# Optimization experiments

Hardware: AMD Instinct MI355X
Metric: run time of the kernel (lower is better)

Reference implementation:

```python
import jax, jax.numpy as jnp
import numpy as np
import math

N_EMBD = 2048
N_HEAD = 16
HEAD_DIM = N_EMBD // N_HEAD
B, T = 2, 2048


def setup_inputs() -> dict:
    key = jax.random.key(0)
    k1, k2, k3 = jax.random.split(key, 3)
    x = jax.random.normal(k1, (B, T, N_EMBD), dtype=jnp.float32)
    # Linear weights stored torch-style [out, in]; applied as x @ W.T
    W_gate = jax.random.normal(k2, (N_HEAD, N_EMBD), dtype=jnp.float32) * 0.02
    W_qkv = jax.random.normal(k3, (3 * N_EMBD, N_EMBD), dtype=jnp.float32) * 0.02
    return {"x": x, "W_gate": W_gate, "W_qkv": W_qkv}


def reference(x, W_gate, W_qkv):
    Bb, Tt, C = x.shape
    H, hd = N_HEAD, HEAD_DIM
    # --- top-1 head gating ---
    gating = jax.nn.softmax(x @ W_gate.T, axis=-1)            # [B,T,H]
    idx = jnp.argmax(gating, axis=-1)                          # [B,T]
    indicator = jax.nn.one_hot(idx, H, dtype=gating.dtype)     # [B,T,H] (no grad, like scatter of ones)
    top1_val = jnp.max(gating, axis=-1, keepdims=True)         # [B,T,1]
    gating_top1 = indicator * top1_val                         # [B,T,H]
    # --- qkv projection ---
    qkv = x @ W_qkv.T                                          # [B,T,3C]
    q, k, v = jnp.split(qkv, 3, axis=-1)
    k = k.reshape(Bb, Tt, H, hd)
    v = v.reshape(Bb, Tt, H, hd)
    # scatter-style weighted collapse of heads -> single shared K/V head (MQA)
    k_shared = jnp.einsum('bth,bthd->btd', indicator, k)       # [B,T,hd]
    v_shared = jnp.einsum('bth,bthd->btd', gating_top1, v)     # [B,T,hd]
    q = q.reshape(Bb, Tt, H, hd).transpose(0, 2, 1, 3)         # [B,H,T,hd]
    # --- causal softmax attention (materialized, as in source) ---
    att = jnp.einsum('bhqd,bkd->bhqk', q, k_shared) * (1.0 / math.sqrt(hd))
    causal = jnp.tril(jnp.ones((Tt, Tt), dtype=bool))          # [T,T]
    att = jnp.where(causal[None, None, :, :], att, -jnp.inf)
    att = jax.nn.softmax(att, axis=-1)
    y = jnp.einsum('bhqk,bkd->bhqd', att, v_shared)            # [B,H,T,hd]
    y = y.transpose(0, 2, 1, 3).reshape(Bb, Tt, C)
    return y
```

## Files before the change

### kernel.cpp

```cpp
#include <hip/hip_runtime.h>
#include <math.h>
#include <cstddef>

#define BB 2
#define TT 2048
#define CC 2048
#define HH 16
#define HD 128
#define MM (BB * TT)
#define QKV_N 6144
#define BK 32

typedef __attribute__((ext_vector_type(8))) short short8;
typedef __attribute__((ext_vector_type(4))) float f32x4;

__device__ __forceinline__ unsigned short f2bf(float f) {
    union { float f; unsigned int u; } v; v.f = f;
    unsigned int r = v.u + 0x7FFFu + ((v.u >> 16) & 1u);
    return (unsigned short)(r >> 16);
}
__device__ __forceinline__ unsigned short f2bf_up(float f) {
    union { float f; unsigned int u; } v; v.f = f;
    return (unsigned short)((v.u + 0x8000u) >> 16);
}
__device__ __forceinline__ float bf2f(unsigned short s) {
    union { unsigned int u; float f; } v; v.u = ((unsigned int)s) << 16;
    return v.f;
}
__device__ __forceinline__ void gload16(const void* g, void* l) {
    __builtin_amdgcn_global_load_lds(
        (const __attribute__((address_space(1))) unsigned int*)g,
        (__attribute__((address_space(3))) unsigned int*)l, 16, 0, 0);
}

__global__ __launch_bounds__(256) void gate_convert(const float* __restrict__ x,
                                                    const float* __restrict__ Wg,
                                                    int* __restrict__ idxbuf,
                                                    float* __restrict__ top1buf,
                                                    unsigned short* __restrict__ xb,
                                                    const float* __restrict__ Wqkv,
                                                    unsigned short* __restrict__ wb) {
    int tid = threadIdx.x;
    if (blockIdx.x >= 4096) {
        int i = (blockIdx.x - 4096) * 256 + tid;
        int n8 = QKV_N * CC / 8;
        if (i >= n8) return;
        const float4* s4 = (const float4*)Wqkv;
        float4 a = s4[i * 2], b = s4[i * 2 + 1];
        union { unsigned short s[8]; uint4 u; } pk;
        pk.s[0] = f2bf(a.x); pk.s[1] = f2bf(a.y); pk.s[2] = f2bf(a.z); pk.s[3] = f2bf(a.w);
        pk.s[4] = f2bf(b.x); pk.s[5] = f2bf(b.y); pk.s[6] = f2bf(b.z); pk.s[7] = f2bf(b.w);
        ((uint4*)wb)[i] = pk.u;
        return;
    }
    int m = blockIdx.x;
    int h = tid >> 4;
    int j = tid & 15;
    const float4* xr = (const float4*)(x + (size_t)m * CC);
    const float4* wr = (const float4*)(Wg + (size_t)h * CC);
    float acc = 0.f;
#pragma unroll 8
    for (int i = 0; i < CC / 4; i += 16) {
        float4 a = xr[i + j];
        float4 b = wr[i + j];
        acc += a.x * b.x + a.y * b.y + a.z * b.z + a.w * b.w;
    }
    for (int off = 8; off > 0; off >>= 1) acc += __shfl_down(acc, off, 16);
    __shared__ float logits[HH];
    if (j == 0) logits[h] = acc;
    {
        float4 a = xr[tid * 2], b = xr[tid * 2 + 1];
        union { unsigned short s[8]; uint4 u; } pk;
        pk.s[0] = f2bf(a.x); pk.s[1] = f2bf(a.y); pk.s[2] = f2bf(a.z); pk.s[3] = f2bf(a.w);
        pk.s[4] = f2bf(b.x); pk.s[5] = f2bf(b.y); pk.s[6] = f2bf(b.z); pk.s[7] = f2bf(b.w);
        ((uint4*)(xb + (size_t)m * CC))[tid] = pk.u;
    }
    __syncthreads();
    if (tid == 0) {
        float zmax = logits[0];
        int best = 0;
        for (int i = 1; i < HH; i++) {
            if (logits[i] > zmax) { zmax = logits[i]; best = i; }
        }
        float s = 0.f;
        for (int i = 0; i < HH; i++) s += expf(logits[i] - zmax);
        idxbuf[m] = best;
        top1buf[m] = 1.0f / s;
    }
}

__global__ __launch_bounds__(256) void bucket_kernel(const int* __restrict__ idxb,
                                                     int* __restrict__ ord,
                                                     int* __restrict__ hs) {
    __shared__ unsigned short cnts[256][16];
    __shared__ int hsum[16], hbase[16];
    int t = threadIdx.x;
    unsigned short c[16];
#pragma unroll
    for (int h = 0; h < 16; h++) c[h] = 0;
    int hv[16];
#pragma unroll
    for (int i = 0; i < 16; i++) {
        hv[i] = idxb[t * 16 + i];
        c[hv[i]]++;
    }
#pragma unroll
    for (int h = 0; h < 16; h++) cnts[t][h] = c[h];
    __syncthreads();
    if (t < 16) {
        int s = 0;
        for (int j = 0; j < 256; j++) {
            int v = cnts[j][t];
            cnts[j][t] = (unsigned short)s;
            s += v;
        }
        hsum[t] = s;
    }
    __syncthreads();
    if (t == 0) {
        int s = 0;
        for (int h = 0; h < 16; h++) { hbase[h] = s; hs[h] = s; s += hsum[h]; }
        hs[16] = s;
    }
    __syncthreads();
    int pos[16];
#pragma unroll
    for (int h = 0; h < 16; h++) pos[h] = hbase[h] + (int)cnts[t][h];
#pragma unroll
    for (int i = 0; i < 16; i++) {
        int h = hv[i];
        ord[pos[h]++] = t * 16 + i;
    }
}

__global__ __launch_bounds__(256) void qkv_gemm(const unsigned short* __restrict__ A,
                                                const unsigned short* __restrict__ Bm,
                                                unsigned short* __restrict__ C,
                                                const int* __restrict__ ord,
                                                const int* __restrict__ hs,
                                                const float* __restrict__ top1,
                                                unsigned short* __restrict__ kshB,
                                                unsigned short* __restrict__ vshT) {
    __shared__ unsigned short ShA[2][128 * BK];
    __shared__ unsigned short ShB[2][128 * BK];
    int tid = threadIdx.x;
    int wave = tid >> 6, lane = tid & 63;
    int l = lane & 15, g = lane >> 4;
    int flat = blockIdx.x;

    if (flat < 512) {
        int m0 = (flat >> 4) * 128, n0 = (flat & 15) * 128;
        int wr = wave >> 1, wc = wave & 1;

        f32x4 acc[4][4];
#pragma unroll
        for (int i = 0; i < 4; i++)
#pragma unroll
            for (int j = 0; j < 4; j++) acc[i][j] = (f32x4){0.f, 0.f, 0.f, 0.f};

        int srow = lane >> 2;
        int scol = (lane & 3) * 8;
        const unsigned short* aB0 = A + (size_t)(m0 + wave * 32 + srow) * 2048 + scol;
        const unsigned short* bB0 = Bm + (size_t)(n0 + wave * 32 + srow) * 2048 + scol;

#define QSTAGE(k0_, bi) do {                                                    \
        gload16(aB0 + (k0_), &ShA[bi][wave * 1024]);                            \
        gload16(aB0 + (k0_) + (size_t)16 * 2048, &ShA[bi][wave * 1024 + 512]);  \
        gload16(bB0 + (k0_), &ShB[bi][wave * 1024]);                            \
        gload16(bB0 + (k0_) + (size_t)16 * 2048, &ShB[bi][wave * 1024 + 512]);  \
    } while (0)

        QSTAGE(0, 0);
        __syncthreads();

        for (int k0 = 0; k0 < 2048; k0 += BK) {
            int cur = (k0 >> 5) & 1;
            if (k0 + BK < 2048) QSTAGE(k0 + BK, cur ^ 1);
            short8 af[4], bf[4];
#pragma unroll
            for (int i = 0; i < 4; i++)
                af[i] = *(const short8*)&ShA[cur][(wr * 64 + i * 16 + l) * BK + g * 8];
#pragma unroll
            for (int j = 0; j < 4; j++)
                bf[j] = *(const short8*)&ShB[cur][(wc * 64 + j * 16 + l) * BK + g * 8];
#pragma unroll
            for (int i = 0; i < 4; i++)
#pragma unroll
                for (int j = 0; j < 4; j++)
                    acc[i][j] = __builtin_amdgcn_mfma_f32_16x16x32_bf16(af[i], bf[j], acc[i][j], 0, 0, 0);
            __syncthreads();
        }
#undef QSTAGE

        const float qscale = 0.08838834764831845f;
#pragma unroll
        for (int j = 0; j < 4; j++) {
            int col = n0 + wc * 64 + j * 16 + l;
#pragma unroll
            for (int i = 0; i < 4; i++) {
                int row = m0 + wr * 64 + i * 16 + g * 4;
#pragma unroll
                for (int r = 0; r < 4; r++)
                    C[(size_t)(row + r) * CC + col] = f2bf(acc[i][j][r] * qscale);
            }
        }
        return;
    }

    {
        int kv = flat - 512;
        int h = kv & 15, reg = (kv >> 4) & 1, mt = kv >> 5;
        int s0 = hs[h], s1 = hs[h + 1];
        int cnt = s1 - s0;
        if (mt * 64 >= cnt) return;
        int base = s0 + mt * 64;

        int arow = base + wave * 16 + (lane >> 2);
        int atok = ord[(arow < s1) ? arow : (s1 - 1)];
        const unsigned short* aSrc = A + (size_t)atok * CC + (lane & 3) * 8;
        int wr0 = 2048 + reg * 2048 + h * 128;
        const unsigned short* bSrc0 = Bm + (size_t)(wr0 + (wave * 2 + 0) * 16 + (lane >> 2)) * CC + (lane & 3) * 8;
        const unsigned short* bSrc1 = Bm + (size_t)(wr0 + (wave * 2 + 1) * 16 + (lane >> 2)) * CC + (lane & 3) * 8;

#define KSTAGE(k0_, bi) do {                                      \
        gload16(aSrc + (k0_), &ShA[bi][wave * 512]);              \
        gload16(bSrc0 + (k0_), &ShB[bi][(wave * 2 + 0) * 512]);   \
        gload16(bSrc1 + (k0_), &ShB[bi][(wave * 2 + 1) * 512]);   \
    } while (0)

        f32x4 acc[8];
#pragma unroll
        for (int j = 0; j < 8; j++) acc[j] = (f32x4){0.f, 0.f, 0.f, 0.f};

        KSTAGE(0, 0);
        __syncthreads();

        for (int k0 = 0; k0 < 2048; k0 += 32) {
            int cur = (k0 >> 5) & 1;
            if (k0 + 32 < 2048) KSTAGE(k0 + 32, cur ^ 1);
            short8 af = *(const short8*)&ShA[cur][(wave * 16 + l) * 32 + g * 8];
#pragma unroll
            for (int j = 0; j < 8; j++) {
                short8 bf = *(const short8*)&ShB[cur][(j * 16 + l) * 32 + g * 8];
                acc[j] = __builtin_amdgcn_mfma_f32_16x16x32_bf16(af, bf, acc[j], 0, 0, 0);
            }
            __syncthreads();
        }
#undef KSTAGE

#pragma unroll
        for (int i = 0; i < 4; i++) {
            int r = wave * 16 + g * 4 + i;
            if (base + r >= s1) continue;
            int tok = ord[base + r];
            if (reg == 0) {
#pragma unroll
                for (int j = 0; j < 8; j++)
                    kshB[(size_t)tok * HD + j * 16 + l] = f2bf(acc[j][i]);
            } else {
                float tv = top1[tok];
#pragma unroll
                for (int j = 0; j < 8; j++)
                    vshT[(size_t)(j * 16 + l) * MM + tok] = f2bf(acc[j][i] * tv);
            }
        }
    }
}

__global__ __launch_bounds__(256, 4) void attn_mfma(const unsigned short* __restrict__ qb,
                                                    const unsigned short* __restrict__ kb,
                                                    const unsigned short* __restrict__ vtb,
                                                    float* __restrict__ y) {
    __shared__ unsigned short KsA[2][32 * 128];
    __shared__ unsigned short VtA[2][128 * 32];
    __shared__ unsigned short Ps[4][16][40];

    int bid = blockIdx.x;
    int t = bid & 255, r = bid >> 8;
    int k = (r << 8) | ((r & 1) ? (255 - t) : t);
    int qi = 127 - (k >> 3);
    int b  = (k >> 2) & 1;
    int hq = k & 3;
    int q0 = qi * 16;
    int nch = (qi >> 1) + 1;
    int tid = threadIdx.x;
    int wave = tid >> 6;
    int lane = tid & 63;
    int l = lane & 15;
    int g = lane >> 4;
    int h = hq * 4 + wave;

    short8 qf[4];
    {
        const unsigned short* qrow = qb + (size_t)(b * TT + q0 + l) * CC + h * HD;
#pragma unroll
        for (int kc = 0; kc < 4; kc++)
            qf[kc] = *(const short8*)(qrow + kc * 32 + g * 8);
    }

    short8 onesf;
    {
        short v = (l == 0) ? (short)0x3F80 : (short)0;
#pragma unroll
        for (int e = 0; e < 8; e++) onesf[e] = v;
    }

    f32x4 o[8];
    f32x4 o8 = (f32x4){0.f, 0.f, 0.f, 0.f};
#pragma unroll
    for (int n = 0; n < 8; n++) o[n] = (f32x4){0.f, 0.f, 0.f, 0.f};

    const unsigned short* kbase = kb + (size_t)b * TT * HD;
    int rbase = q0 + g * 4;

#define STAGE(cc, bufi) do {                                                      \
        int kc0_ = (cc) * 32;                                                     \
        _Pragma("unroll")                                                         \
        for (int rep_ = 0; rep_ < 2; rep_++) {                                    \
            int s_ = tid + rep_ * 256;                                            \
            int kr_ = s_ >> 4, kp_ = s_ & 15;                                     \
            gload16(kbase + (size_t)(kc0_ + kr_) * HD + ((kp_ ^ (kr_ & 15)) * 8), \
                    &KsA[bufi][(rep_ * 256 + wave * 64) * 8]);                    \
            int vd_ = s_ >> 2, vp_ = s_ & 3;                                      \
            int vq_ = vp_ ^ ((vd_ >> 1) & 3);                                     \
            gload16(vtb + (size_t)vd_ * MM + b * TT + kc0_ + vq_ * 8,             \
                    &VtA[bufi][(rep_ * 256 + wave * 64) * 8]);                    \
        }                                                                         \
    } while (0)

    STAGE(0, 0);
    __syncthreads();

    for (int c = 0; c < nch; c++) {
        int kc0 = c * 32;
        int cur = c & 1;
        if (c + 1 < nch) STAGE(c + 1, cur ^ 1);
        bool diag = (c == nch - 1);
        const unsigned short* Kc = KsA[cur];
        const unsigned short* Vc = VtA[cur];

#pragma unroll
        for (int tt = 0; tt < 2; tt++) {
            short8 kf[4];
#pragma unroll
            for (int kc = 0; kc < 4; kc++)
                kf[kc] = *(const short8*)&Kc[(tt * 16 + l) * 128 + (((kc * 4 + g) ^ l) * 8)];
            f32x4 sl = (f32x4){0.f, 0.f, 0.f, 0.f};
#pragma unroll
            for (int kc = 0; kc < 4; kc++)
                sl = __builtin_amdgcn_mfma_f32_16x16x32_bf16(qf[kc], kf[kc], sl, 0, 0, 0);
            if (diag) {
                int key = kc0 + tt * 16 + l;
#pragma unroll
                for (int i = 0; i < 4; i++)
                    if (key > rbase + i) sl[i] = -1e30f;
            }
#pragma unroll
            for (int i = 0; i < 4; i++)
                Ps[wave][g * 4 + i][tt * 16 + l] = f2bf_up(__expf(sl[i] - 30.f));
        }
        {
            short8 pf0 = *(const short8*)&Ps[wave][l][g * 8];
#pragma unroll
            for (int n = 0; n < 8; n++) {
                short8 vf = *(const short8*)&Vc[(n * 16 + l) * 32 + ((g ^ ((l >> 1) & 3)) * 8)];
                o[n] = __builtin_amdgcn_mfma_f32_16x16x32_bf16(pf0, vf, o[n], 0, 0, 0);
            }
            o8 = __builtin_amdgcn_mfma_f32_16x16x32_bf16(pf0, onesf, o8, 0, 0, 0);
        }
        __syncthreads();
    }
#undef STAGE

    {
        float inv[4];
#pragma unroll
        for (int i = 0; i < 4; i++) {
            float lv = __shfl(o8[i], lane & 48);
            inv[i] = 1.f / lv;
        }
#pragma unroll
        for (int n = 0; n < 8; n++) {
#pragma unroll
            for (int i = 0; i < 4; i++) {
                y[(size_t)(b * TT + q0 + g * 4 + i) * CC + h * HD + n * 16 + l] =
                    o[n][i] * inv[i];
            }
        }
    }
}

extern "C" void kernel_launch(void* const* d_in, const int* in_sizes, int n_in,
                              void* d_out, int out_size, void* d_ws, size_t ws_size,
                              hipStream_t stream) {
    (void)in_sizes; (void)n_in; (void)out_size; (void)ws_size;
    const float* x    = (const float*)d_in[0];
    const float* Wg   = (const float*)d_in[1];
    const float* Wqkv = (const float*)d_in[2];
    float* y = (float*)d_out;

    unsigned short* xb   = (unsigned short*)d_ws;
    unsigned short* wb   = xb + (size_t)MM * CC;
    unsigned short* qbuf = wb + (size_t)QKV_N * CC;
    unsigned short* kshB = qbuf + (size_t)MM * CC;
    unsigned short* vshT = kshB + (size_t)MM * HD;
    float* top1 = (float*)(vshT + (size_t)HD * MM);
    int*   idxb = (int*)(top1 + MM);
    int*   ord  = idxb + MM;
    int*   hs   = ord + MM;

    gate_convert<<<4096 + 6144, 256, 0, stream>>>(x, Wg, idxb, top1, xb, Wqkv, wb);
    bucket_kernel<<<1, 256, 0, stream>>>(idxb, ord, hs);
    qkv_gemm<<<512 + 2048, 256, 0, stream>>>(xb, wb, qbuf, ord, hs, top1, kshB, vshT);
    attn_mfma<<<1024, 256, 0, stream>>>(qbuf, kshB, vshT, y);
}
```

Measured before the change: 279.6 us.

## Fuse bucket sort into gate kernel via last-block atomic; add MFMA setprio

Removes the separate single-block bucket_kernel launch. Each gating block now increments a global counter after writing its result, and the last block to finish runs the histogram, prefix sum and scatter of token order inside gate_convert. A memset of the counter is added before the launch. Separately, the attention kernel raises wave priority around its MFMA sequences so matrix work is issued ahead of other waves. The cost is an extra atomic and fence per block, more shared memory in gate_convert, and a serial tail in whichever block finishes last.

```diff
diff --git a/kernel.cpp b/kernel.cpp
--- a/kernel.cpp
+++ b/kernel.cpp
@@ -39,12 +39,13 @@
                                                     float* __restrict__ top1buf,
                                                     unsigned short* __restrict__ xb,
                                                     const float* __restrict__ Wqkv,
-                                                    unsigned short* __restrict__ wb) {
+                                                    unsigned short* __restrict__ wb,
+                                                    int* __restrict__ ord,
+                                                    int* __restrict__ hs,
+                                                    int* __restrict__ cnt) {
     int tid = threadIdx.x;
     if (blockIdx.x >= 4096) {
         int i = (blockIdx.x - 4096) * 256 + tid;
-        int n8 = QKV_N * CC / 8;
-        if (i >= n8) return;
         const float4* s4 = (const float4*)Wqkv;
         float4 a = s4[i * 2], b = s4[i * 2 + 1];
         union { unsigned short s[8]; uint4 u; } pk;
@@ -53,6 +54,10 @@
         ((uint4*)wb)[i] = pk.u;
         return;
     }
+    __shared__ float logits[HH];
+    __shared__ int amLast;
+    __shared__ unsigned short cnts[256][16];
+    __shared__ int hsum[16], hbase[16];
     int m = blockIdx.x;
     int h = tid >> 4;
     int j = tid & 15;
@@ -66,7 +71,6 @@
         acc += a.x * b.x + a.y * b.y + a.z * b.z + a.w * b.w;
     }
     for (int off = 8; off > 0; off >>= 1) acc += __shfl_down(acc, off, 16);
-    __shared__ float logits[HH];
     if (j == 0) logits[h] = acc;
     {
         float4 a = xr[tid * 2], b = xr[tid * 2 + 1];
@@ -86,50 +90,51 @@
         for (int i = 0; i < HH; i++) s += expf(logits[i] - zmax);
         idxbuf[m] = best;
         top1buf[m] = 1.0f / s;
-    }
-}
-
-__global__ __launch_bounds__(256) void bucket_kernel(const int* __restrict__ idxb,
-                                                     int* __restrict__ ord,
-                                                     int* __restrict__ hs) {
-    __shared__ unsigned short cnts[256][16];
-    __shared__ int hsum[16], hbase[16];
-    int t = threadIdx.x;
-    unsigned short c[16];
-#pragma unroll
-    for (int h = 0; h < 16; h++) c[h] = 0;
-    int hv[16];
-#pragma unroll
-    for (int i = 0; i < 16; i++) {
-        hv[i] = idxb[t * 16 + i];
-        c[hv[i]]++;
-    }
-#pragma unroll
-    for (int h = 0; h < 16; h++) cnts[t][h] = c[h];
+        __threadfence();
+        int old = atomicAdd(cnt, 1);
+        amLast = (old == 4095);
+    }
     __syncthreads();
-    if (t < 16) {
-        int s = 0;
-        for (int j = 0; j < 256; j++) {
-            int v = cnts[j][t];
-            cnts[j][t] = (unsigned short)s;
-            s += v;
-        }
-        hsum[t] = s;
-    }
-    __syncthreads();
-    if (t == 0) {
-        int s = 0;
-        for (int h = 0; h < 16; h++) { hbase[h] = s; hs[h] = s; s += hsum[h]; }
-        hs[16] = s;
-    }
-    __syncthreads();
-    int pos[16];
-#pragma unroll
-    for (int h = 0; h < 16; h++) pos[h] = hbase[h] + (int)cnts[t][h];
-#pragma unroll
-    for (int i = 0; i < 16; i++) {
-        int h = hv[i];
-        ord[pos[h]++] = t * 16 + i;
+    if (!amLast) return;
+    __threadfence();
+    {
+        int t = tid;
+        unsigned short c[16];
+#pragma unroll
+        for (int hh = 0; hh < 16; hh++) c[hh] = 0;
+        int hv[16];
+#pragma unroll
+        for (int i = 0; i < 16; i++) {
+            hv[i] = idxbuf[t * 16 + i];
+            c[hv[i]]++;
+        }
+#pragma unroll
+        for (int hh = 0; hh < 16; hh++) cnts[t][hh] = c[hh];
+        __syncthreads();
+        if (t < 16) {
+            int s = 0;
+            for (int jj = 0; jj < 256; jj++) {
+                int v = cnts[jj][t];
+                cnts[jj][t] = (unsigned short)s;
+                s += v;
+            }
+            hsum[t] = s;
+        }
+        __syncthreads();
+        if (t == 0) {
+            int s = 0;
+            for (int hh = 0; hh < 16; hh++) { hbase[hh] = s; hs[hh] = s; s += hsum[hh]; }
+            hs[16] = s;
+        }
+        __syncthreads();
+        int pos[16];
+#pragma unroll
+        for (int hh = 0; hh < 16; hh++) pos[hh] = hbase[hh] + (int)cnts[t][hh];
+#pragma unroll
+        for (int i = 0; i < 16; i++) {
+            int hh = hv[i];
+            ord[pos[hh]++] = t * 16 + i;
+        }
     }
 }
 
@@ -346,9 +351,11 @@
             for (int kc = 0; kc < 4; kc++)
                 kf[kc] = *(const short8*)&Kc[(tt * 16 + l) * 128 + (((kc * 4 + g) ^ l) * 8)];
             f32x4 sl = (f32x4){0.f, 0.f, 0.f, 0.f};
+            __builtin_amdgcn_s_setprio(1);
 #pragma unroll
             for (int kc = 0; kc < 4; kc++)
                 sl = __builtin_amdgcn_mfma_f32_16x16x32_bf16(qf[kc], kf[kc], sl, 0, 0, 0);
+            __builtin_amdgcn_s_setprio(0);
             if (diag) {
                 int key = kc0 + tt * 16 + l;
 #pragma unroll
@@ -361,12 +368,14 @@
         }
         {
             short8 pf0 = *(const short8*)&Ps[wave][l][g * 8];
+            __builtin_amdgcn_s_setprio(1);
 #pragma unroll
             for (int n = 0; n < 8; n++) {
                 short8 vf = *(const short8*)&Vc[(n * 16 + l) * 32 + ((g ^ ((l >> 1) & 3)) * 8)];
                 o[n] = __builtin_amdgcn_mfma_f32_16x16x32_bf16(pf0, vf, o[n], 0, 0, 0);
             }
             o8 = __builtin_amdgcn_mfma_f32_16x16x32_bf16(pf0, onesf, o8, 0, 0, 0);
+            __builtin_amdgcn_s_setprio(0);
         }
         __syncthreads();
     }
@@ -408,9 +417,10 @@
     int*   idxb = (int*)(top1 + MM);
     int*   ord  = idxb + MM;
     int*   hs   = ord + MM;
-
-    gate_convert<<<4096 + 6144, 256, 0, stream>>>(x, Wg, idxb, top1, xb, Wqkv, wb);
-    bucket_kernel<<<1, 256, 0, stream>>>(idxb, ord, hs);
+    int*   cntr = hs + 17;
+
+    hipMemsetAsync(cntr, 0, 4, stream);
+    gate_convert<<<4096 + 6144, 256, 0, stream>>>(x, Wg, idxb, top1, xb, Wqkv, wb, ord, hs, cntr);
     qkv_gemm<<<512 + 2048, 256, 0, stream>>>(xb, wb, qbuf, ord, hs, top1, kshB, vshT);
     attn_mfma<<<1024, 256, 0, stream>>>(qbuf, kshB, vshT, y);
 }
```

Result: slower. 434.5 us (+55.4%).
